# Performance work log

Measured on AMD Instinct MI355X. Metric: run time of the kernel, lower is better.

The kernel has to match this reference:

```python
import jax, jax.numpy as jnp
import numpy as np
from functools import partial

HEAD_DIM = 64
KERNEL_SIZE = 3
TOPK = KERNEL_SIZE * KERNEL_SIZE  # 9 selected keys per query
SCALE = HEAD_DIM ** (-0.5)        # note: original code DIVIDES by this scale


def setup_inputs() -> dict:
    key = jax.random.key(0)
    k1, k2, k3 = jax.random.split(key, 3)
    B, d, H, W = 4, HEAD_DIM, 96, 96
    q = jax.random.normal(k1, (B, d, H, W), dtype=jnp.float32)
    k = jax.random.normal(k2, (B, d, H, W), dtype=jnp.float32)
    v = jax.random.normal(k3, (B, d, H, W), dtype=jnp.float32)
    return {"q": q, "k": k, "v": v}


def reference(q, k, v):
    B, d, H, W = q.shape
    N = H * W
    # [B, d, H, W] -> [B, N, d]
    qf = q.reshape(B, d, N).transpose(0, 2, 1)
    kf = k.reshape(B, d, N).transpose(0, 2, 1)
    vf = v.reshape(B, d, N).transpose(0, 2, 1)
    # dense scores [B, N, N]; original divides by scale (= head_dim**-0.5)
    attn = jnp.einsum('bnd,bmd->bnm', qf, kf) / SCALE
    # top-k key selection per query
    sel, idx = jax.lax.top_k(attn, TOPK)          # [B, N, K], [B, N, K]
    w = jax.nn.softmax(sel, axis=-1)              # [B, N, K]
    # gather selected values: [B, N, K, d]
    sel_v = vf[jnp.arange(B)[:, None, None], idx]
    # weighted sum over the K selected keys
    x = jnp.einsum('bnk,bnkd->bnd', w, sel_v)     # [B, N, d]
    return x.reshape(B, H, W, d)
```

## Files before the change

kernel.cpp:

```cpp
#include <hip/hip_runtime.h>
#include <math.h>

#define HD     64
#define NPIX   9216
#define B4     4
#define NQ     (B4 * NPIX)
#define K9     9
#define SSL    8
#define ZS     16
#define KQZ    (NPIX / ZS)
#define KTG    64
#define NTG    (KQZ / KTG)
#define KTS    32
#define NTS    9
#define DGATE  13.0f
#define CAP    96

typedef __attribute__((ext_vector_type(8)))  short bf16x8;
typedef __attribute__((ext_vector_type(16))) float f32x16;
typedef unsigned short ushort_t;
typedef unsigned long long u64;

__device__ __forceinline__ ushort_t f2bf(float x) {
  unsigned u = __float_as_uint(x);
  unsigned r = (u + 0x7fffu + ((u >> 16) & 1u)) >> 16;
  return (ushort_t)r;
}

__global__ __launch_bounds__(256) void prep_kernel(
    const float* __restrict__ qg, const float* __restrict__ kg,
    const float* __restrict__ vg,
    ushort_t* __restrict__ Qbf, ushort_t* __restrict__ Kbf,
    float* __restrict__ Kt, float* __restrict__ Vt, int* __restrict__ Cnt) {
  __shared__ float Ts[64][65];
  const int b = blockIdx.y, n0 = blockIdx.x * 64, z = blockIdx.z;
  const float* src = (z == 0) ? qg : (z == 1) ? kg : vg;
  const int tid = threadIdx.x;
  if (z == 0 && b == 0) Cnt[blockIdx.x * 256 + tid] = 0;
  #pragma unroll
  for (int i = 0; i < 16; ++i) {
    const int idx = i * 256 + tid, c = idx >> 6, nl = idx & 63;
    Ts[c][nl] = src[((size_t)b * HD + c) * NPIX + n0 + nl];
  }
  __syncthreads();
  if (z == 0) {
    #pragma unroll
    for (int i = 0; i < 16; ++i) {
      const int idx = i * 256 + tid, nl = idx >> 6, d = idx & 63;
      Qbf[((size_t)b * NPIX + n0 + nl) * HD + d] = f2bf(Ts[d][nl] * 8.f);
    }
  } else if (z == 1) {
    #pragma unroll
    for (int i = 0; i < 16; ++i) {
      const int idx = i * 256 + tid, nl = idx >> 6, d = idx & 63;
      const float x = Ts[d][nl];
      const size_t o = ((size_t)b * NPIX + n0 + nl) * HD + d;
      Kbf[o] = f2bf(x); Kt[o] = x;
    }
  } else {
    #pragma unroll
    for (int i = 0; i < 16; ++i) {
      const int idx = i * 256 + tid, nl = idx >> 6, d = idx & 63;
      Vt[((size_t)b * NPIX + n0 + nl) * HD + d] = Ts[d][nl];
    }
  }
}

__device__ __forceinline__ void gl_lds16(const void* g, void* l) {
  auto gp = reinterpret_cast<const unsigned int __attribute__((address_space(1)))*>(
      reinterpret_cast<uintptr_t>(g));
  auto lp = reinterpret_cast<unsigned int __attribute__((address_space(3)))*>(
      reinterpret_cast<uintptr_t>(l));
  __builtin_amdgcn_global_load_lds(gp, lp, 16, 0, 0);
}

__global__ __launch_bounds__(256, 4) void pass_sample(
    const ushort_t* __restrict__ Qbf, const ushort_t* __restrict__ Kbf,
    float* __restrict__ Pm) {
  __shared__ __align__(16) char SM[2][4096];

  const int tid = threadIdx.x;
  const int w = tid >> 6, l = tid & 63;
  const int lq = l & 31, hi = l >> 5, par = l & 7;
  const int b = blockIdx.y, qbase = blockIdx.x * 256, z = blockIdx.z;
  const int kbase = z * KTS * NTS;
  const int qw = qbase + w * 64;

  bf16x8 qf0[4], qf1[4];
  {
    const size_t q0 = ((size_t)b * NPIX + qw + lq) * HD + hi * 8;
    const size_t q1 = q0 + (size_t)32 * HD;
    #pragma unroll
    for (int i = 0; i < 4; ++i) {
      qf0[i] = *reinterpret_cast<const bf16x8*>(Qbf + q0 + i * 16);
      qf1[i] = *reinterpret_cast<const bf16x8*>(Qbf + q1 + i * 16);
    }
  }

  const char* kB = reinterpret_cast<const char*>(Kbf + (size_t)b * NPIX * HD);
  const int sr = tid >> 3, sc = tid & 7;
  const int srcoff = sr * 128 + ((sc ^ (sr & 7)) << 4);
  const int hdst = w * 1024;
  int oi[4];
  #pragma unroll
  for (int i = 0; i < 4; ++i) oi[i] = lq * 128 + (((i * 2 + hi) ^ par) << 4);

  auto stage = [&](int tile, int nb) {
    const size_t toff = ((size_t)(kbase + tile * KTS)) * 128 + srcoff;
    gl_lds16(kB + toff, SM[nb] + hdst);
  };

  float m0 = -3.4e38f, m1 = -3.4e38f;
  stage(0, 0);
  __syncthreads();

  for (int t = 0; t < NTS; ++t) {
    const int cur = t & 1;
    if (t + 1 < NTS) stage(t + 1, cur ^ 1);
    const char* kt = SM[cur];

    f32x16 a0 = {0.f,0.f,0.f,0.f,0.f,0.f,0.f,0.f,0.f,0.f,0.f,0.f,0.f,0.f,0.f,0.f};
    f32x16 a1 = {0.f,0.f,0.f,0.f,0.f,0.f,0.f,0.f,0.f,0.f,0.f,0.f,0.f,0.f,0.f,0.f};
    #pragma unroll
    for (int i = 0; i < 4; ++i) {
      const bf16x8 av = *reinterpret_cast<const bf16x8*>(kt + oi[i]);
      a0 = __builtin_amdgcn_mfma_f32_32x32x16_bf16(av, qf0[i], a0, 0, 0, 0);
      a1 = __builtin_amdgcn_mfma_f32_32x32x16_bf16(av, qf1[i], a1, 0, 0, 0);
    }
    float s0 = fmaxf(fmaxf(fmaxf(a0[0],a0[1]),fmaxf(a0[2],a0[3])),
               fmaxf(fmaxf(a0[4],a0[5]),fmaxf(a0[6],a0[7])));
    s0 = fmaxf(s0, fmaxf(fmaxf(fmaxf(a0[8],a0[9]),fmaxf(a0[10],a0[11])),
                   fmaxf(fmaxf(a0[12],a0[13]),fmaxf(a0[14],a0[15]))));
    float s1 = fmaxf(fmaxf(fmaxf(a1[0],a1[1]),fmaxf(a1[2],a1[3])),
               fmaxf(fmaxf(a1[4],a1[5]),fmaxf(a1[6],a1[7])));
    s1 = fmaxf(s1, fmaxf(fmaxf(fmaxf(a1[8],a1[9]),fmaxf(a1[10],a1[11])),
                   fmaxf(fmaxf(a1[12],a1[13]),fmaxf(a1[14],a1[15]))));
    m0 = fmaxf(m0, s0);
    m1 = fmaxf(m1, s1);
    __syncthreads();
  }

  m0 = fmaxf(m0, __shfl_xor(m0, 32, 64));
  m1 = fmaxf(m1, __shfl_xor(m1, 32, 64));
  if (l < 32) {
    Pm[(size_t)z * NQ + b * NPIX + qw + l]      = m0;
    Pm[(size_t)z * NQ + b * NPIX + qw + 32 + l] = m1;
  }
}

struct LB { u64 lo, hi; int cnt; };

__device__ __forceinline__ void flushLB(LB& b, int qi, int kbase,
                                        int* __restrict__ Cnt,
                                        unsigned* __restrict__ Cand) {
  if (b.cnt == 0) return;
  const int slot = atomicAdd(&Cnt[qi], b.cnt);
  for (int j = 0; j < b.cnt; ++j) {
    const int sh = 16 * j;
    const unsigned key = (sh < 64) ? (unsigned)((b.lo >> sh) & 0xFFFFull)
                                   : (unsigned)((b.hi >> (sh - 64)) & 0xFFFFull);
    if (slot + j < CAP)
      Cand[(size_t)qi * CAP + slot + j] = (unsigned)(kbase + (int)key);
  }
  b.lo = 0ull; b.hi = 0ull; b.cnt = 0;
}

__device__ __forceinline__ void pushLB(LB& b, unsigned key10, int qi, int kbase,
                                       int* __restrict__ Cnt,
                                       unsigned* __restrict__ Cand) {
  b.hi = (b.hi << 16) | (b.lo >> 48);
  b.lo = (b.lo << 16) | (u64)key10;
  if (++b.cnt == 8) flushLB(b, qi, kbase, Cnt, Cand);
}

__global__ __launch_bounds__(256, 4) void pass_gate(
    const ushort_t* __restrict__ Qbf, const ushort_t* __restrict__ Kbf,
    const float* __restrict__ Pm,
    int* __restrict__ Cnt, unsigned* __restrict__ Cand) {
  __shared__ __align__(16) char SM[2][8192];

  const int tid = threadIdx.x;
  const int w = tid >> 6, l = tid & 63;
  const int lq = l & 31, hi = l >> 5, par = l & 7;
  const int b = blockIdx.y, qbase = blockIdx.x * 256, z = blockIdx.z;
  const int kbase = z * KQZ;
  const int qw = qbase + w * 64;

  const int qi0 = b * NPIX + qw + lq;
  const int qi1 = qi0 + 32;

  bf16x8 qf0[4], qf1[4];
  {
    const size_t q0 = (size_t)qi0 * HD + hi * 8;
    const size_t q1 = (size_t)qi1 * HD + hi * 8;
    #pragma unroll
    for (int i = 0; i < 4; ++i) {
      qf0[i] = *reinterpret_cast<const bf16x8*>(Qbf + q0 + i * 16);
      qf1[i] = *reinterpret_cast<const bf16x8*>(Qbf + q1 + i * 16);
    }
  }

  float tau0 = -3.4e38f, tau1 = -3.4e38f;
  #pragma unroll
  for (int s = 0; s < SSL; ++s) {
    tau0 = fmaxf(tau0, Pm[(size_t)s * NQ + qi0]);
    tau1 = fmaxf(tau1, Pm[(size_t)s * NQ + qi1]);
  }
  float gt0 = tau0 - DGATE, gt1 = tau1 - DGATE;

  const char* kB = reinterpret_cast<const char*>(Kbf + (size_t)b * NPIX * HD);
  const int sr = tid >> 3, sc = tid & 7;
  const int srcoff = sr * 128 + ((sc ^ (sr & 7)) << 4);
  const int hdst = w * 1024;
  int oi[4];
  #pragma unroll
  for (int i = 0; i < 4; ++i) oi[i] = lq * 128 + (((i * 2 + hi) ^ par) << 4);

  auto stage = [&](int tile, int nb) {
    const size_t toff = ((size_t)(kbase + tile * KTG)) * 128 + srcoff;
    gl_lds16(kB + toff, SM[nb] + hdst);
    gl_lds16(kB + toff + 4096, SM[nb] + 4096 + hdst);
  };

  LB lb0 = {0ull, 0ull, 0}, lb1 = {0ull, 0ull, 0};

  auto chain = [&](const f32x16& a, float& gt, LB& lb, int qi, int kb) {
    const float t0 = fmaxf(fmaxf(a[0],  a[1]),  a[2]);
    const float t1 = fmaxf(fmaxf(a[3],  a[4]),  a[5]);
    const float t2 = fmaxf(fmaxf(a[6],  a[7]),  a[8]);
    const float t3 = fmaxf(fmaxf(a[9],  a[10]), a[11]);
    const float t4 = fmaxf(fmaxf(a[12], a[13]), a[14]);
    const float s16 = fmaxf(fmaxf(fmaxf(t0, t1), t2),
                            fmaxf(fmaxf(t3, t4), a[15]));
    const float old = gt;
    gt = fmaxf(old, s16 - DGATE);
    if (s16 > old) {
      #pragma unroll
      for (int e = 0; e < 16; ++e) {
        const int off = (e >> 2) * 8 + (e & 3);
        if (a[e] > gt) pushLB(lb, (unsigned)(kb + off), qi, kbase, Cnt, Cand);
      }
    }
  };

  stage(0, 0);
  __syncthreads();

  for (int t = 0; t < NTG; ++t) {
    const int cur = t & 1;
    if (t + 1 < NTG) stage(t + 1, cur ^ 1);
    const char* kt = SM[cur];

    #pragma unroll
    for (int g = 0; g < 2; ++g) {
      const int gbyte = g * 4096;
      f32x16 a0 = {0.f,0.f,0.f,0.f,0.f,0.f,0.f,0.f,0.f,0.f,0.f,0.f,0.f,0.f,0.f,0.f};
      f32x16 a1 = {0.f,0.f,0.f,0.f,0.f,0.f,0.f,0.f,0.f,0.f,0.f,0.f,0.f,0.f,0.f,0.f};
      #pragma unroll
      for (int i = 0; i < 4; ++i) {
        const bf16x8 av = *reinterpret_cast<const bf16x8*>(kt + gbyte + oi[i]);
        a0 = __builtin_amdgcn_mfma_f32_32x32x16_bf16(av, qf0[i], a0, 0, 0, 0);
        a1 = __builtin_amdgcn_mfma_f32_32x32x16_bf16(av, qf1[i], a1, 0, 0, 0);
      }
      const int kb = t * KTG + g * 32 + 4 * hi;
      chain(a0, gt0, lb0, qi0, kb);
      chain(a1, gt1, lb1, qi1, kb);
    }
    __syncthreads();
  }

  flushLB(lb0, qi0, kbase, Cnt, Cand);
  flushLB(lb1, qi1, kbase, Cnt, Cand);
}

__global__ __launch_bounds__(256) void merge_v(
    const unsigned* __restrict__ Cand, const int* __restrict__ Cnt,
    const float* __restrict__ qg, const float* __restrict__ Kt,
    const float* __restrict__ Vt, float* __restrict__ Og) {
  __shared__ float Qs[8][HD];
  const int tid = threadIdx.x, b = blockIdx.y;
  const int nbase = blockIdx.x * 8;

  {
    const int ql = tid >> 5, d0 = (tid & 31) * 2;
    const int n = nbase + ql;
    Qs[ql][d0]     = 8.f * qg[((size_t)b * HD + d0) * NPIX + n];
    Qs[ql][d0 + 1] = 8.f * qg[((size_t)b * HD + d0 + 1) * NPIX + n];
  }
  __syncthreads();

  const int wid = tid >> 6, lane = tid & 63;
  const int half = lane >> 5, l32 = lane & 31;
  const int ql = wid * 2 + half;
  const int n  = nbase + ql;
  const int qi = b * NPIX + n;
  const int c  = min(Cnt[qi], CAP);

  u64 p[3] = {0ull, 0ull, 0ull};
  #pragma unroll
  for (int r = 0; r < 3; ++r) {
    const int j = r * 32 + l32;
    if (j < c) {
      const int idx = (int)Cand[(size_t)qi * CAP + j];
      const float4* kr = reinterpret_cast<const float4*>(
          Kt + ((size_t)b * NPIX + idx) * HD);
      float acc = 0.f;
      #pragma unroll
      for (int u = 0; u < 16; ++u) {
        const float4 qx = *reinterpret_cast<const float4*>(&Qs[ql][u * 4]);
        const float4 kx = kr[u];
        acc = fmaf(qx.x, kx.x, acc); acc = fmaf(qx.y, kx.y, acc);
        acc = fmaf(qx.z, kx.z, acc); acc = fmaf(qx.w, kx.w, acc);
      }
      unsigned ub = __float_as_uint(acc);
      ub = (ub & 0x80000000u) ? ~ub : (ub | 0x80000000u);
      p[r] = ((u64)ub << 14) | (u64)(unsigned)(0x3FFF - idx);
    }
  }

  float mv[K9]; int mi[K9];
  #pragma unroll
  for (int r = 0; r < K9; ++r) {
    u64 bst = p[0] > p[1] ? p[0] : p[1];
    bst = bst > p[2] ? bst : p[2];
    #pragma unroll
    for (int m = 1; m < 32; m <<= 1) {
      const u64 o = __shfl_xor(bst, m, 32);
      bst = (o > bst) ? o : bst;
    }
    if (bst != 0ull) {
      #pragma unroll
      for (int s = 0; s < 3; ++s) if (p[s] == bst) p[s] = 0ull;
      const int idx = 0x3FFF - (int)(bst & 0x3FFFull);
      unsigned ub = (unsigned)(bst >> 14);
      ub = (ub & 0x80000000u) ? (ub ^ 0x80000000u) : ~ub;
      mv[r] = __uint_as_float(ub);
      mi[r] = idx;
    } else {
      mv[r] = -3.4e38f; mi[r] = 0;
    }
  }

  const float mmax = mv[0];
  float wr[K9]; float wsum = 0.f;
  #pragma unroll
  for (int r = 0; r < K9; ++r) { wr[r] = expf(mv[r] - mmax); wsum += wr[r]; }
  const float inv = 1.f / wsum;

  float2 o2 = make_float2(0.f, 0.f);
  #pragma unroll
  for (int r = 0; r < K9; ++r) {
    const float w2 = wr[r] * inv;
    const float2 v2 = *reinterpret_cast<const float2*>(
        Vt + ((size_t)b * NPIX + mi[r]) * HD + l32 * 2);
    o2.x = fmaf(w2, v2.x, o2.x);
    o2.y = fmaf(w2, v2.y, o2.y);
  }
  *reinterpret_cast<float2*>(Og + ((size_t)b * NPIX + n) * HD + l32 * 2) = o2;
}

extern "C" void kernel_launch(void* const* d_in, const int* in_sizes, int n_in,
                              void* d_out, int out_size, void* d_ws, size_t ws_size,
                              hipStream_t stream) {
  const float* q = (const float*)d_in[0];
  const float* k = (const float*)d_in[1];
  const float* v = (const float*)d_in[2];
  float* o = (float*)d_out;

  const size_t asz = (size_t)B4 * NPIX * HD;
  ushort_t* Qbf = (ushort_t*)d_ws;
  ushort_t* Kbf = Qbf + asz;
  float*    Kt  = (float*)(Kbf + asz);
  float*    Vt  = Kt + asz;
  float*    Pm  = Vt + asz;
  int*      Ct  = (int*)(Pm + (size_t)SSL * NQ);
  unsigned* Cd  = (unsigned*)(Ct + NQ);

  prep_kernel<<<dim3(NPIX / 64, B4, 3), 256, 0, stream>>>(q, k, v, Qbf, Kbf, Kt, Vt, Ct);
  pass_sample<<<dim3(NPIX / 256, B4, SSL), 256, 0, stream>>>(Qbf, Kbf, Pm);
  pass_gate<<<dim3(NPIX / 256, B4, ZS), 256, 0, stream>>>(Qbf, Kbf, Pm, Ct, Cd);
  merge_v<<<dim3(NPIX / 8, B4), 256, 0, stream>>>(Cd, Ct, q, Kt, Vt, o);
}
```

Baseline: 124.0 us.

## Halve queries per wave in sample and gate passes to raise occupancy

After: 129.8 us. +4.7%, slower.

```diff
diff --git a/kernel.cpp b/kernel.cpp
--- a/kernel.cpp
+++ b/kernel.cpp
@@ -74,7 +74,7 @@
   __builtin_amdgcn_global_load_lds(gp, lp, 16, 0, 0);
 }
 
-__global__ __launch_bounds__(256, 4) void pass_sample(
+__global__ __launch_bounds__(256, 8) void pass_sample(
     const ushort_t* __restrict__ Qbf, const ushort_t* __restrict__ Kbf,
     float* __restrict__ Pm) {
   __shared__ __align__(16) char SM[2][4096];
@@ -82,19 +82,17 @@
   const int tid = threadIdx.x;
   const int w = tid >> 6, l = tid & 63;
   const int lq = l & 31, hi = l >> 5, par = l & 7;
-  const int b = blockIdx.y, qbase = blockIdx.x * 256, z = blockIdx.z;
+  const int b = blockIdx.y, qbase = blockIdx.x * 128, z = blockIdx.z;
   const int kbase = z * KTS * NTS;
-  const int qw = qbase + w * 64;
-
-  bf16x8 qf0[4], qf1[4];
+  const int qw = qbase + w * 32;
+  const int qi = b * NPIX + qw + lq;
+
+  bf16x8 qf[4];
   {
-    const size_t q0 = ((size_t)b * NPIX + qw + lq) * HD + hi * 8;
-    const size_t q1 = q0 + (size_t)32 * HD;
-    #pragma unroll
-    for (int i = 0; i < 4; ++i) {
-      qf0[i] = *reinterpret_cast<const bf16x8*>(Qbf + q0 + i * 16);
-      qf1[i] = *reinterpret_cast<const bf16x8*>(Qbf + q1 + i * 16);
-    }
+    const size_t q0 = (size_t)qi * HD + hi * 8;
+    #pragma unroll
+    for (int i = 0; i < 4; ++i)
+      qf[i] = *reinterpret_cast<const bf16x8*>(Qbf + q0 + i * 16);
   }
 
   const char* kB = reinterpret_cast<const char*>(Kbf + (size_t)b * NPIX * HD);
@@ -110,7 +108,7 @@
     gl_lds16(kB + toff, SM[nb] + hdst);
   };
 
-  float m0 = -3.4e38f, m1 = -3.4e38f;
+  float m = -3.4e38f;
   stage(0, 0);
   __syncthreads();
 
@@ -119,33 +117,23 @@
     if (t + 1 < NTS) stage(t + 1, cur ^ 1);
     const char* kt = SM[cur];
 
-    f32x16 a0 = {0.f,0.f,0.f,0.f,0.f,0.f,0.f,0.f,0.f,0.f,0.f,0.f,0.f,0.f,0.f,0.f};
-    f32x16 a1 = {0.f,0.f,0.f,0.f,0.f,0.f,0.f,0.f,0.f,0.f,0.f,0.f,0.f,0.f,0.f,0.f};
+    f32x16 a = {0.f,0.f,0.f,0.f,0.f,0.f,0.f,0.f,0.f,0.f,0.f,0.f,0.f,0.f,0.f,0.f};
     #pragma unroll
     for (int i = 0; i < 4; ++i) {
       const bf16x8 av = *reinterpret_cast<const bf16x8*>(kt + oi[i]);
-      a0 = __builtin_amdgcn_mfma_f32_32x32x16_bf16(av, qf0[i], a0, 0, 0, 0);
-      a1 = __builtin_amdgcn_mfma_f32_32x32x16_bf16(av, qf1[i], a1, 0, 0, 0);
-    }
-    float s0 = fmaxf(fmaxf(fmaxf(a0[0],a0[1]),fmaxf(a0[2],a0[3])),
-               fmaxf(fmaxf(a0[4],a0[5]),fmaxf(a0[6],a0[7])));
-    s0 = fmaxf(s0, fmaxf(fmaxf(fmaxf(a0[8],a0[9]),fmaxf(a0[10],a0[11])),
-                   fmaxf(fmaxf(a0[12],a0[13]),fmaxf(a0[14],a0[15]))));
-    float s1 = fmaxf(fmaxf(fmaxf(a1[0],a1[1]),fmaxf(a1[2],a1[3])),
-               fmaxf(fmaxf(a1[4],a1[5]),fmaxf(a1[6],a1[7])));
-    s1 = fmaxf(s1, fmaxf(fmaxf(fmaxf(a1[8],a1[9]),fmaxf(a1[10],a1[11])),
-                   fmaxf(fmaxf(a1[12],a1[13]),fmaxf(a1[14],a1[15]))));
-    m0 = fmaxf(m0, s0);
-    m1 = fmaxf(m1, s1);
+      a = __builtin_amdgcn_mfma_f32_32x32x16_bf16(av, qf[i], a, 0, 0, 0);
+    }
+    const float t0 = fmaxf(fmaxf(a[0],  a[1]),  a[2]);
+    const float t1 = fmaxf(fmaxf(a[3],  a[4]),  a[5]);
+    const float t2 = fmaxf(fmaxf(a[6],  a[7]),  a[8]);
+    const float t3 = fmaxf(fmaxf(a[9],  a[10]), a[11]);
+    const float t4 = fmaxf(fmaxf(a[12], a[13]), a[14]);
+    m = fmaxf(m, fmaxf(fmaxf(fmaxf(t0, t1), t2), fmaxf(fmaxf(t3, t4), a[15])));
     __syncthreads();
   }
 
-  m0 = fmaxf(m0, __shfl_xor(m0, 32, 64));
-  m1 = fmaxf(m1, __shfl_xor(m1, 32, 64));
-  if (l < 32) {
-    Pm[(size_t)z * NQ + b * NPIX + qw + l]      = m0;
-    Pm[(size_t)z * NQ + b * NPIX + qw + 32 + l] = m1;
-  }
+  m = fmaxf(m, __shfl_xor(m, 32, 64));
+  if (l < 32) Pm[(size_t)z * NQ + qi] = m;
 }
 
 struct LB { u64 lo, hi; int cnt; };
@@ -173,7 +161,7 @@
   if (++b.cnt == 8) flushLB(b, qi, kbase, Cnt, Cand);
 }
 
-__global__ __launch_bounds__(256, 4) void pass_gate(
+__global__ __launch_bounds__(256, 8) void pass_gate(
     const ushort_t* __restrict__ Qbf, const ushort_t* __restrict__ Kbf,
     const float* __restrict__ Pm,
     int* __restrict__ Cnt, unsigned* __restrict__ Cand) {
@@ -182,31 +170,23 @@
   const int tid = threadIdx.x;
   const int w = tid >> 6, l = tid & 63;
   const int lq = l & 31, hi = l >> 5, par = l & 7;
-  const int b = blockIdx.y, qbase = blockIdx.x * 256, z = blockIdx.z;
+  const int b = blockIdx.y, qbase = blockIdx.x * 128, z = blockIdx.z;
   const int kbase = z * KQZ;
-  const int qw = qbase + w * 64;
-
-  const int qi0 = b * NPIX + qw + lq;
-  const int qi1 = qi0 + 32;
-
-  bf16x8 qf0[4], qf1[4];
+  const int qw = qbase + w * 32;
+  const int qi = b * NPIX + qw + lq;
+
+  bf16x8 qf[4];
   {
-    const size_t q0 = (size_t)qi0 * HD + hi * 8;
-    const size_t q1 = (size_t)qi1 * HD + hi * 8;
-    #pragma unroll
-    for (int i = 0; i < 4; ++i) {
-      qf0[i] = *reinterpret_cast<const bf16x8*>(Qbf + q0 + i * 16);
-      qf1[i] = *reinterpret_cast<const bf16x8*>(Qbf + q1 + i * 16);
-    }
-  }
-
-  float tau0 = -3.4e38f, tau1 = -3.4e38f;
-  #pragma unroll
-  for (int s = 0; s < SSL; ++s) {
-    tau0 = fmaxf(tau0, Pm[(size_t)s * NQ + qi0]);
-    tau1 = fmaxf(tau1, Pm[(size_t)s * NQ + qi1]);
-  }
-  float gt0 = tau0 - DGATE, gt1 = tau1 - DGATE;
+    const size_t q0 = (size_t)qi * HD + hi * 8;
+    #pragma unroll
+    for (int i = 0; i < 4; ++i)
+      qf[i] = *reinterpret_cast<const bf16x8*>(Qbf + q0 + i * 16);
+  }
+
+  float tau = -3.4e38f;
+  #pragma unroll
+  for (int s = 0; s < SSL; ++s) tau = fmaxf(tau, Pm[(size_t)s * NQ + qi]);
+  float gt = tau - DGATE;
 
   const char* kB = reinterpret_cast<const char*>(Kbf + (size_t)b * NPIX * HD);
   const int sr = tid >> 3, sc = tid & 7;
@@ -222,26 +202,7 @@
     gl_lds16(kB + toff + 4096, SM[nb] + 4096 + hdst);
   };
 
-  LB lb0 = {0ull, 0ull, 0}, lb1 = {0ull, 0ull, 0};
-
-  auto chain = [&](const f32x16& a, float& gt, LB& lb, int qi, int kb) {
-    const float t0 = fmaxf(fmaxf(a[0],  a[1]),  a[2]);
-    const float t1 = fmaxf(fmaxf(a[3],  a[4]),  a[5]);
-    const float t2 = fmaxf(fmaxf(a[6],  a[7]),  a[8]);
-    const float t3 = fmaxf(fmaxf(a[9],  a[10]), a[11]);
-    const float t4 = fmaxf(fmaxf(a[12], a[13]), a[14]);
-    const float s16 = fmaxf(fmaxf(fmaxf(t0, t1), t2),
-                            fmaxf(fmaxf(t3, t4), a[15]));
-    const float old = gt;
-    gt = fmaxf(old, s16 - DGATE);
-    if (s16 > old) {
-      #pragma unroll
-      for (int e = 0; e < 16; ++e) {
-        const int off = (e >> 2) * 8 + (e & 3);
-        if (a[e] > gt) pushLB(lb, (unsigned)(kb + off), qi, kbase, Cnt, Cand);
-      }
-    }
-  };
+  LB lb = {0ull, 0ull, 0};
 
   stage(0, 0);
   __syncthreads();
@@ -254,23 +215,34 @@
     #pragma unroll
     for (int g = 0; g < 2; ++g) {
       const int gbyte = g * 4096;
-      f32x16 a0 = {0.f,0.f,0.f,0.f,0.f,0.f,0.f,0.f,0.f,0.f,0.f,0.f,0.f,0.f,0.f,0.f};
-      f32x16 a1 = {0.f,0.f,0.f,0.f,0.f,0.f,0.f,0.f,0.f,0.f,0.f,0.f,0.f,0.f,0.f,0.f};
+      f32x16 a = {0.f,0.f,0.f,0.f,0.f,0.f,0.f,0.f,0.f,0.f,0.f,0.f,0.f,0.f,0.f,0.f};
       #pragma unroll
       for (int i = 0; i < 4; ++i) {
         const bf16x8 av = *reinterpret_cast<const bf16x8*>(kt + gbyte + oi[i]);
-        a0 = __builtin_amdgcn_mfma_f32_32x32x16_bf16(av, qf0[i], a0, 0, 0, 0);
-        a1 = __builtin_amdgcn_mfma_f32_32x32x16_bf16(av, qf1[i], a1, 0, 0, 0);
+        a = __builtin_amdgcn_mfma_f32_32x32x16_bf16(av, qf[i], a, 0, 0, 0);
       }
-      const int kb = t * KTG + g * 32 + 4 * hi;
-      chain(a0, gt0, lb0, qi0, kb);
-      chain(a1, gt1, lb1, qi1, kb);
+      const float t0 = fmaxf(fmaxf(a[0],  a[1]),  a[2]);
+      const float t1 = fmaxf(fmaxf(a[3],  a[4]),  a[5]);
+      const float t2 = fmaxf(fmaxf(a[6],  a[7]),  a[8]);
+      const float t3 = fmaxf(fmaxf(a[9],  a[10]), a[11]);
+      const float t4 = fmaxf(fmaxf(a[12], a[13]), a[14]);
+      const float s16 = fmaxf(fmaxf(fmaxf(t0, t1), t2),
+                              fmaxf(fmaxf(t3, t4), a[15]));
+      const float old = gt;
+      gt = fmaxf(old, s16 - DGATE);
+      if (s16 > old) {
+        const int kb = t * KTG + g * 32 + 4 * hi;
+        #pragma unroll
+        for (int e = 0; e < 16; ++e) {
+          const int off = (e >> 2) * 8 + (e & 3);
+          if (a[e] > gt) pushLB(lb, (unsigned)(kb + off), qi, kbase, Cnt, Cand);
+        }
+      }
     }
     __syncthreads();
   }
 
-  flushLB(lb0, qi0, kbase, Cnt, Cand);
-  flushLB(lb1, qi1, kbase, Cnt, Cand);
+  flushLB(lb, qi, kbase, Cnt, Cand);
 }
 
 __global__ __launch_bounds__(256) void merge_v(
@@ -377,7 +349,7 @@
   unsigned* Cd  = (unsigned*)(Ct + NQ);
 
   prep_kernel<<<dim3(NPIX / 64, B4, 3), 256, 0, stream>>>(q, k, v, Qbf, Kbf, Kt, Vt, Ct);
-  pass_sample<<<dim3(NPIX / 256, B4, SSL), 256, 0, stream>>>(Qbf, Kbf, Pm);
-  pass_gate<<<dim3(NPIX / 256, B4, ZS), 256, 0, stream>>>(Qbf, Kbf, Pm, Ct, Cd);
+  pass_sample<<<dim3(NPIX / 128, B4, SSL), 256, 0, stream>>>(Qbf, Kbf, Pm);
+  pass_gate<<<dim3(NPIX / 128, B4, ZS), 256, 0, stream>>>(Qbf, Kbf, Pm, Ct, Cd);
   merge_v<<<dim3(NPIX / 8, B4), 256, 0, stream>>>(Cd, Ct, q, Kt, Vt, o);
 }
```

## Shrink sample and gate passes to single-wave blocks with per-wave K staging

Applied to the files above, without the earlier changes.

After: 127.8 us. +3.1%, slower.

```diff
diff --git a/kernel.cpp b/kernel.cpp
--- a/kernel.cpp
+++ b/kernel.cpp
@@ -9,9 +9,8 @@
 #define SSL    8
 #define ZS     16
 #define KQZ    (NPIX / ZS)
-#define KTG    64
-#define NTG    (KQZ / KTG)
-#define KTS    32
+#define KTL    32
+#define NTG    (KQZ / KTL)
 #define NTS    9
 #define DGATE  13.0f
 #define CAP    96
@@ -72,80 +71,6 @@
   auto lp = reinterpret_cast<unsigned int __attribute__((address_space(3)))*>(
       reinterpret_cast<uintptr_t>(l));
   __builtin_amdgcn_global_load_lds(gp, lp, 16, 0, 0);
-}
-
-__global__ __launch_bounds__(256, 4) void pass_sample(
-    const ushort_t* __restrict__ Qbf, const ushort_t* __restrict__ Kbf,
-    float* __restrict__ Pm) {
-  __shared__ __align__(16) char SM[2][4096];
-
-  const int tid = threadIdx.x;
-  const int w = tid >> 6, l = tid & 63;
-  const int lq = l & 31, hi = l >> 5, par = l & 7;
-  const int b = blockIdx.y, qbase = blockIdx.x * 256, z = blockIdx.z;
-  const int kbase = z * KTS * NTS;
-  const int qw = qbase + w * 64;
-
-  bf16x8 qf0[4], qf1[4];
-  {
-    const size_t q0 = ((size_t)b * NPIX + qw + lq) * HD + hi * 8;
-    const size_t q1 = q0 + (size_t)32 * HD;
-    #pragma unroll
-    for (int i = 0; i < 4; ++i) {
-      qf0[i] = *reinterpret_cast<const bf16x8*>(Qbf + q0 + i * 16);
-      qf1[i] = *reinterpret_cast<const bf16x8*>(Qbf + q1 + i * 16);
-    }
-  }
-
-  const char* kB = reinterpret_cast<const char*>(Kbf + (size_t)b * NPIX * HD);
-  const int sr = tid >> 3, sc = tid & 7;
-  const int srcoff = sr * 128 + ((sc ^ (sr & 7)) << 4);
-  const int hdst = w * 1024;
-  int oi[4];
-  #pragma unroll
-  for (int i = 0; i < 4; ++i) oi[i] = lq * 128 + (((i * 2 + hi) ^ par) << 4);
-
-  auto stage = [&](int tile, int nb) {
-    const size_t toff = ((size_t)(kbase + tile * KTS)) * 128 + srcoff;
-    gl_lds16(kB + toff, SM[nb] + hdst);
-  };
-
-  float m0 = -3.4e38f, m1 = -3.4e38f;
-  stage(0, 0);
-  __syncthreads();
-
-  for (int t = 0; t < NTS; ++t) {
-    const int cur = t & 1;
-    if (t + 1 < NTS) stage(t + 1, cur ^ 1);
-    const char* kt = SM[cur];
-
-    f32x16 a0 = {0.f,0.f,0.f,0.f,0.f,0.f,0.f,0.f,0.f,0.f,0.f,0.f,0.f,0.f,0.f,0.f};
-    f32x16 a1 = {0.f,0.f,0.f,0.f,0.f,0.f,0.f,0.f,0.f,0.f,0.f,0.f,0.f,0.f,0.f,0.f};
-    #pragma unroll
-    for (int i = 0; i < 4; ++i) {
-      const bf16x8 av = *reinterpret_cast<const bf16x8*>(kt + oi[i]);
-      a0 = __builtin_amdgcn_mfma_f32_32x32x16_bf16(av, qf0[i], a0, 0, 0, 0);
-      a1 = __builtin_amdgcn_mfma_f32_32x32x16_bf16(av, qf1[i], a1, 0, 0, 0);
-    }
-    float s0 = fmaxf(fmaxf(fmaxf(a0[0],a0[1]),fmaxf(a0[2],a0[3])),
-               fmaxf(fmaxf(a0[4],a0[5]),fmaxf(a0[6],a0[7])));
-    s0 = fmaxf(s0, fmaxf(fmaxf(fmaxf(a0[8],a0[9]),fmaxf(a0[10],a0[11])),
-                   fmaxf(fmaxf(a0[12],a0[13]),fmaxf(a0[14],a0[15]))));
-    float s1 = fmaxf(fmaxf(fmaxf(a1[0],a1[1]),fmaxf(a1[2],a1[3])),
-               fmaxf(fmaxf(a1[4],a1[5]),fmaxf(a1[6],a1[7])));
-    s1 = fmaxf(s1, fmaxf(fmaxf(fmaxf(a1[8],a1[9]),fmaxf(a1[10],a1[11])),
-                   fmaxf(fmaxf(a1[12],a1[13]),fmaxf(a1[14],a1[15]))));
-    m0 = fmaxf(m0, s0);
-    m1 = fmaxf(m1, s1);
-    __syncthreads();
-  }
-
-  m0 = fmaxf(m0, __shfl_xor(m0, 32, 64));
-  m1 = fmaxf(m1, __shfl_xor(m1, 32, 64));
-  if (l < 32) {
-    Pm[(size_t)z * NQ + b * NPIX + qw + l]      = m0;
-    Pm[(size_t)z * NQ + b * NPIX + qw + 32 + l] = m1;
-  }
 }
 
 struct LB { u64 lo, hi; int cnt; };
@@ -173,19 +98,15 @@
   if (++b.cnt == 8) flushLB(b, qi, kbase, Cnt, Cand);
 }
 
-__global__ __launch_bounds__(256, 4) void pass_gate(
+__global__ __launch_bounds__(64, 4) void pass_sample(
     const ushort_t* __restrict__ Qbf, const ushort_t* __restrict__ Kbf,
-    const float* __restrict__ Pm,
-    int* __restrict__ Cnt, unsigned* __restrict__ Cand) {
-  __shared__ __align__(16) char SM[2][8192];
-
-  const int tid = threadIdx.x;
-  const int w = tid >> 6, l = tid & 63;
-  const int lq = l & 31, hi = l >> 5, par = l & 7;
-  const int b = blockIdx.y, qbase = blockIdx.x * 256, z = blockIdx.z;
-  const int kbase = z * KQZ;
-  const int qw = qbase + w * 64;
-
+    float* __restrict__ Pm) {
+  __shared__ __align__(16) char SM[2][4096];
+
+  const int l = threadIdx.x;
+  const int lq = l & 31, hi = l >> 5, par = lq & 7;
+  const int b = blockIdx.y, qw = blockIdx.x * 64, z = blockIdx.z;
+  const int kbase = z * KTL * NTS;
   const int qi0 = b * NPIX + qw + lq;
   const int qi1 = qi0 + 32;
 
@@ -200,6 +121,90 @@
     }
   }
 
+  const char* kB = reinterpret_cast<const char*>(Kbf + (size_t)b * NPIX * HD);
+  const int sr = l >> 3, sc = l & 7;
+  const int srcoff = sr * 128 + ((sc ^ sr) << 4);
+  int oi[4];
+  #pragma unroll
+  for (int i = 0; i < 4; ++i) oi[i] = lq * 128 + (((i * 2 + hi) ^ par) << 4);
+
+  auto stage = [&](int tile, int nb) {
+    const size_t toff = ((size_t)(kbase + tile * KTL)) * 128 + srcoff;
+    #pragma unroll
+    for (int p = 0; p < 4; ++p)
+      gl_lds16(kB + toff + p * 1024, SM[nb] + p * 1024);
+  };
+
+  float m0 = -3.4e38f, m1 = -3.4e38f;
+  stage(0, 0);
+
+  for (int t = 0; t < NTS; ++t) {
+    const int cur = t & 1;
+    if (t + 1 < NTS) stage(t + 1, cur ^ 1);
+    __syncthreads();
+    const char* kt = SM[cur];
+
+    f32x16 a0 = {0.f,0.f,0.f,0.f,0.f,0.f,0.f,0.f,0.f,0.f,0.f,0.f,0.f,0.f,0.f,0.f};
+    f32x16 a1 = {0.f,0.f,0.f,0.f,0.f,0.f,0.f,0.f,0.f,0.f,0.f,0.f,0.f,0.f,0.f,0.f};
+    #pragma unroll
+    for (int i = 0; i < 4; ++i) {
+      const bf16x8 av = *reinterpret_cast<const bf16x8*>(kt + oi[i]);
+      a0 = __builtin_amdgcn_mfma_f32_32x32x16_bf16(av, qf0[i], a0, 0, 0, 0);
+      a1 = __builtin_amdgcn_mfma_f32_32x32x16_bf16(av, qf1[i], a1, 0, 0, 0);
+    }
+    {
+      const float t0 = fmaxf(fmaxf(a0[0],  a0[1]),  a0[2]);
+      const float t1 = fmaxf(fmaxf(a0[3],  a0[4]),  a0[5]);
+      const float t2 = fmaxf(fmaxf(a0[6],  a0[7]),  a0[8]);
+      const float t3 = fmaxf(fmaxf(a0[9],  a0[10]), a0[11]);
+      const float t4 = fmaxf(fmaxf(a0[12], a0[13]), a0[14]);
+      m0 = fmaxf(m0, fmaxf(fmaxf(fmaxf(t0, t1), t2),
+                           fmaxf(fmaxf(t3, t4), a0[15])));
+    }
+    {
+      const float t0 = fmaxf(fmaxf(a1[0],  a1[1]),  a1[2]);
+      const float t1 = fmaxf(fmaxf(a1[3],  a1[4]),  a1[5]);
+      const float t2 = fmaxf(fmaxf(a1[6],  a1[7]),  a1[8]);
+      const float t3 = fmaxf(fmaxf(a1[9],  a1[10]), a1[11]);
+      const float t4 = fmaxf(fmaxf(a1[12], a1[13]), a1[14]);
+      m1 = fmaxf(m1, fmaxf(fmaxf(fmaxf(t0, t1), t2),
+                           fmaxf(fmaxf(t3, t4), a1[15])));
+    }
+    __syncthreads();
+  }
+
+  m0 = fmaxf(m0, __shfl_xor(m0, 32, 64));
+  m1 = fmaxf(m1, __shfl_xor(m1, 32, 64));
+  if (l < 32) {
+    Pm[(size_t)z * NQ + qi0] = m0;
+    Pm[(size_t)z * NQ + qi1] = m1;
+  }
+}
+
+__global__ __launch_bounds__(64, 4) void pass_gate(
+    const ushort_t* __restrict__ Qbf, const ushort_t* __restrict__ Kbf,
+    const float* __restrict__ Pm,
+    int* __restrict__ Cnt, unsigned* __restrict__ Cand) {
+  __shared__ __align__(16) char SM[2][4096];
+
+  const int l = threadIdx.x;
+  const int lq = l & 31, hi = l >> 5, par = lq & 7;
+  const int b = blockIdx.y, qw = blockIdx.x * 64, z = blockIdx.z;
+  const int kbase = z * KQZ;
+  const int qi0 = b * NPIX + qw + lq;
+  const int qi1 = qi0 + 32;
+
+  bf16x8 qf0[4], qf1[4];
+  {
+    const size_t q0 = (size_t)qi0 * HD + hi * 8;
+    const size_t q1 = (size_t)qi1 * HD + hi * 8;
+    #pragma unroll
+    for (int i = 0; i < 4; ++i) {
+      qf0[i] = *reinterpret_cast<const bf16x8*>(Qbf + q0 + i * 16);
+      qf1[i] = *reinterpret_cast<const bf16x8*>(Qbf + q1 + i * 16);
+    }
+  }
+
   float tau0 = -3.4e38f, tau1 = -3.4e38f;
   #pragma unroll
   for (int s = 0; s < SSL; ++s) {
@@ -209,17 +214,17 @@
   float gt0 = tau0 - DGATE, gt1 = tau1 - DGATE;
 
   const char* kB = reinterpret_cast<const char*>(Kbf + (size_t)b * NPIX * HD);
-  const int sr = tid >> 3, sc = tid & 7;
-  const int srcoff = sr * 128 + ((sc ^ (sr & 7)) << 4);
-  const int hdst = w * 1024;
+  const int sr = l >> 3, sc = l & 7;
+  const int srcoff = sr * 128 + ((sc ^ sr) << 4);
   int oi[4];
   #pragma unroll
   for (int i = 0; i < 4; ++i) oi[i] = lq * 128 + (((i * 2 + hi) ^ par) << 4);
 
   auto stage = [&](int tile, int nb) {
-    const size_t toff = ((size_t)(kbase + tile * KTG)) * 128 + srcoff;
-    gl_lds16(kB + toff, SM[nb] + hdst);
-    gl_lds16(kB + toff + 4096, SM[nb] + 4096 + hdst);
+    const size_t toff = ((size_t)(kbase + tile * KTL)) * 128 + srcoff;
+    #pragma unroll
+    for (int p = 0; p < 4; ++p)
+      gl_lds16(kB + toff + p * 1024, SM[nb] + p * 1024);
   };
 
   LB lb0 = {0ull, 0ull, 0}, lb1 = {0ull, 0ull, 0};
@@ -244,28 +249,24 @@
   };
 
   stage(0, 0);
-  __syncthreads();
 
   for (int t = 0; t < NTG; ++t) {
     const int cur = t & 1;
     if (t + 1 < NTG) stage(t + 1, cur ^ 1);
+    __syncthreads();
     const char* kt = SM[cur];
 
-    #pragma unroll
-    for (int g = 0; g < 2; ++g) {
-      const int gbyte = g * 4096;
-      f32x16 a0 = {0.f,0.f,0.f,0.f,0.f,0.f,0.f,0.f,0.f,0.f,0.f,0.f,0.f,0.f,0.f,0.f};
-      f32x16 a1 = {0.f,0.f,0.f,0.f,0.f,0.f,0.f,0.f,0.f,0.f,0.f,0.f,0.f,0.f,0.f,0.f};
-      #pragma unroll
-      for (int i = 0; i < 4; ++i) {
-        const bf16x8 av = *reinterpret_cast<const bf16x8*>(kt + gbyte + oi[i]);
-        a0 = __builtin_amdgcn_mfma_f32_32x32x16_bf16(av, qf0[i], a0, 0, 0, 0);
-        a1 = __builtin_amdgcn_mfma_f32_32x32x16_bf16(av, qf1[i], a1, 0, 0, 0);
-      }
-      const int kb = t * KTG + g * 32 + 4 * hi;
-      chain(a0, gt0, lb0, qi0, kb);
-      chain(a1, gt1, lb1, qi1, kb);
-    }
+    f32x16 a0 = {0.f,0.f,0.f,0.f,0.f,0.f,0.f,0.f,0.f,0.f,0.f,0.f,0.f,0.f,0.f,0.f};
+    f32x16 a1 = {0.f,0.f,0.f,0.f,0.f,0.f,0.f,0.f,0.f,0.f,0.f,0.f,0.f,0.f,0.f,0.f};
+    #pragma unroll
+    for (int i = 0; i < 4; ++i) {
+      const bf16x8 av = *reinterpret_cast<const bf16x8*>(kt + oi[i]);
+      a0 = __builtin_amdgcn_mfma_f32_32x32x16_bf16(av, qf0[i], a0, 0, 0, 0);
+      a1 = __builtin_amdgcn_mfma_f32_32x32x16_bf16(av, qf1[i], a1, 0, 0, 0);
+    }
+    const int kb = t * KTL + 4 * hi;
+    chain(a0, gt0, lb0, qi0, kb);
+    chain(a1, gt1, lb1, qi1, kb);
     __syncthreads();
   }
 
@@ -377,7 +378,7 @@
   unsigned* Cd  = (unsigned*)(Ct + NQ);
 
   prep_kernel<<<dim3(NPIX / 64, B4, 3), 256, 0, stream>>>(q, k, v, Qbf, Kbf, Kt, Vt, Ct);
-  pass_sample<<<dim3(NPIX / 256, B4, SSL), 256, 0, stream>>>(Qbf, Kbf, Pm);
-  pass_gate<<<dim3(NPIX / 256, B4, ZS), 256, 0, stream>>>(Qbf, Kbf, Pm, Ct, Cd);
+  pass_sample<<<dim3(NPIX / 64, B4, SSL), 64, 0, stream>>>(Qbf, Kbf, Pm);
+  pass_gate<<<dim3(NPIX / 64, B4, ZS), 64, 0, stream>>>(Qbf, Kbf, Pm, Ct, Cd);
   merge_v<<<dim3(NPIX / 8, B4), 256, 0, stream>>>(Cd, Ct, q, Kt, Vt, o);
 }
```
